# Kernel optimization log

Hardware: AMD Instinct MI355X
Metric: run time of the kernel (lower is better)

The kernel has to match this reference:

```python
import jax, jax.numpy as jnp
import numpy as np

B, C, V = 65536, 2, 3          # batch of coords, coord_dim, value_dim
D, K, S = 64, 1024, 4          # latent_dim, num_codes, num_latent_vectors (VQ stages)
H, L, F = 1024, 5, 25          # hidden_size, num_layers, num_freqs
IN = C * (2 * F + 1)           # 102: positional-encoded decoder input
COMMIT = 0.25


def setup_inputs() -> dict:
    key = jax.random.key(0)
    ks = jax.random.split(key, 12)
    coords = jax.random.uniform(ks[0], (B, C), jnp.float32, -1.0, 1.0)
    latents = jax.random.normal(ks[1], (1, S, D), jnp.float32)
    cb = jax.random.normal(ks[2], (S, K, D), jnp.float32)
    codebooks = cb / jnp.linalg.norm(cb, axis=-1, keepdims=True)  # unit-norm init as in module
    mod_W = jax.random.normal(ks[3], (L, D, H), jnp.float32) / np.sqrt(D)
    mod_b = jax.random.normal(ks[4], (L, H), jnp.float32) * 0.01
    dec_W0 = jax.random.normal(ks[5], (IN, H), jnp.float32) / np.sqrt(IN)
    dec_b0 = jax.random.normal(ks[6], (H,), jnp.float32) * 0.01
    dec_Wh = jax.random.normal(ks[7], (L - 1, H, H), jnp.float32) / np.sqrt(H)
    dec_bh = jax.random.normal(ks[8], (L - 1, H), jnp.float32) * 0.01
    dec_Wout = jax.random.normal(ks[9], (H, V), jnp.float32) / np.sqrt(H)
    dec_bout = jax.random.normal(ks[10], (V,), jnp.float32) * 0.01
    return dict(coords=coords, latent_idx=0, latents=latents, codebooks=codebooks,
                mod_W=mod_W, mod_b=mod_b, dec_W0=dec_W0, dec_b0=dec_b0,
                dec_Wh=dec_Wh, dec_bh=dec_bh, dec_Wout=dec_Wout, dec_bout=dec_bout)


def _vq(z, emb):
    # z: (1, D), emb: (K, D) -> squared-distance argmin + straight-through
    d = jnp.sum(z * z, axis=1, keepdims=True) - 2.0 * (z @ emb.T) + jnp.sum(emb * emb, axis=1)
    idx = jnp.argmin(d, axis=1)               # (1,)
    z_q = emb[idx]                            # (1, D)
    z_q_st = z_q + jax.lax.stop_gradient(z - z_q)   # fwd value == z, grad flows to embedding
    loss = COMMIT * jnp.mean((jax.lax.stop_gradient(z_q) - z) ** 2)
    return z_q_st, idx, loss


def reference(coords, latent_idx, latents, codebooks, mod_W, mod_b,
              dec_W0, dec_b0, dec_Wh, dec_bh, dec_Wout, dec_bout):
    img = latents[latent_idx]                 # (S, D)
    z_q_sum = jnp.zeros((1, D), coords.dtype)
    residual_target = jnp.zeros((1, D), coords.dtype)
    total_vq_loss = 0.0
    idxs = []
    for s in range(S):                        # residual VQ over fixed small #stages
        z_stage = img[s:s + 1]
        if s == 0:
            residual_target = z_stage
            z_cur = z_stage
        else:
            residual_target = residual_target + z_stage
            z_cur = residual_target - jax.lax.stop_gradient(z_q_sum)
        z_q_st, idx, l = _vq(z_cur, codebooks[s])
        z_q_sum = z_q_sum + z_q_st
        total_vq_loss = total_vq_loss + l
        idxs.append(idx)
    # modulation betas from the (same-for-all-rows) quantized latent; broadcast over B
    betas = jnp.einsum('od,ldh->loh', z_q_sum, mod_W) + mod_b[:, None, :]   # (L, 1, H)
    # positional encoding: [x, sin(pi*f0*x), cos(pi*f0*x), sin(pi*f1*x), ...]
    freqs = 2.0 ** jnp.arange(F, dtype=coords.dtype)
    ang = coords[:, None, :] * (freqs[None, :, None] * jnp.pi)              # (B, F, C)
    pe = jnp.concatenate(
        [coords, jnp.stack([jnp.sin(ang), jnp.cos(ang)], axis=2).reshape(coords.shape[0], -1)],
        axis=-1)                                                            # (B, IN)
    h = jax.nn.relu(pe @ dec_W0 + dec_b0 + betas[0])
    for i in range(L - 1):
        h = jax.nn.relu(h @ dec_Wh[i] + dec_bh[i] + betas[i + 1])
    values = h @ dec_Wout + dec_bout                                        # (B, V)
    return values, jnp.stack(idxs), total_vq_loss
```

## Files before the change

### kernel.cpp

```cpp
#include <hip/hip_runtime.h>
#include <hip/hip_bf16.h>
#include <stdint.h>

#define NB   65536
#define NC   2
#define NV   3
#define ND   64
#define NK   1024
#define NS   4
#define NH   1024
#define NL   5
#define NF   25
#define NIN  102
#define K0P  128

typedef float f32x4 __attribute__((ext_vector_type(4)));
typedef int   i32x4 __attribute__((ext_vector_type(4)));
typedef int   i32x8 __attribute__((ext_vector_type(8)));
typedef unsigned char u8;

__device__ __forceinline__ void load_lds16(const void* g, void* l) {
    __builtin_amdgcn_global_load_lds(
        (const __attribute__((address_space(1))) void*)g,
        (__attribute__((address_space(3))) void*)l,
        16, 0, 0);
}

__device__ __forceinline__ u8 to_fp8(float x) {
    return (u8)(__builtin_amdgcn_cvt_pk_fp8_f32(x, 0.0f, 0, false) & 0xff);
}


__global__ __launch_bounds__(1024) void vq_kernel(
    const float* __restrict__ latents, const int* __restrict__ latent_idx,
    const float* __restrict__ codebooks, float* __restrict__ zq_out,
    float* __restrict__ out) {
    __shared__ float zcur[ND], resid[ND], zqsum[ND], ssq[ND];
    __shared__ float sDw[16];
    __shared__ int   sKw[16];
    __shared__ int   sBest;
    int t = threadIdx.x, lane = t & 63, wv = t >> 6;
    const float* img = latents + (size_t)latent_idx[0] * (NS * ND);
    if (t < ND) { resid[t] = 0.f; zqsum[t] = 0.f; }
    __syncthreads();
    float lossAcc = 0.f;
    for (int s = 0; s < NS; s++) {
        if (t < ND) {
            float iv = img[s * ND + t];
            float r  = resid[t] + iv;
            resid[t] = r;
            zcur[t]  = (s == 0) ? iv : (r - zqsum[t]);
        }
        __syncthreads();
        float zz = 0.f;
#pragma unroll
        for (int d = 0; d < ND; d++) { float z = zcur[d]; zz += z * z; }
        const float4* e4 = (const float4*)(codebooks + ((size_t)s * NK + t) * ND);
        float dot = 0.f, ee = 0.f;
#pragma unroll
        for (int i = 0; i < 16; i++) {
            float4 v = e4[i];
            dot += zcur[4 * i + 0] * v.x; dot += zcur[4 * i + 1] * v.y;
            dot += zcur[4 * i + 2] * v.z; dot += zcur[4 * i + 3] * v.w;
            ee  += v.x * v.x; ee += v.y * v.y; ee += v.z * v.z; ee += v.w * v.w;
        }
        float dmin = zz - 2.0f * dot + ee;
        int   kmin = t;
#pragma unroll
        for (int m = 1; m < 64; m <<= 1) {
            float d2 = __shfl_xor(dmin, m);
            int   k2 = __shfl_xor(kmin, m);
            if (d2 < dmin || (d2 == dmin && k2 < kmin)) { dmin = d2; kmin = k2; }
        }
        if (lane == 0) { sDw[wv] = dmin; sKw[wv] = kmin; }
        __syncthreads();
        if (t == 0) {
            float bd = sDw[0]; int bk = sKw[0];
            for (int w = 1; w < 16; w++) {
                float d2 = sDw[w]; int k2 = sKw[w];
                if (d2 < bd || (d2 == bd && k2 < bk)) { bd = d2; bk = k2; }
            }
            sBest = bk;
            out[NB * NV + s] = (float)bk;
        }
        __syncthreads();
        int best = sBest;
        const float* eb = codebooks + ((size_t)s * NK + best) * ND;
        if (t < ND) {
            float zq = eb[t];
            float d  = zq - zcur[t];
            ssq[t]   = d * d;
            zqsum[t] = zqsum[t] + (zq + (zcur[t] - zq));
        }
        __syncthreads();
        if (t == 0) {
            float sum = 0.f;
            for (int d = 0; d < ND; d++) sum += ssq[d];
            lossAcc += 0.25f * (sum / (float)ND);
        }
    }
    if (t < ND) zq_out[t] = zqsum[t];
    if (t == 0) out[NB * NV + NS] = lossAcc;
}

__global__ __launch_bounds__(256) void betas_kernel(
    const float* __restrict__ zq, const float* __restrict__ mod_W,
    const float* __restrict__ mod_b, const float* __restrict__ b0,
    const float* __restrict__ bh, float* __restrict__ bb) {
    int g = blockIdx.x * 256 + threadIdx.x;
    int l = g >> 10, n = g & 1023;
    float acc = mod_b[g];
    for (int d = 0; d < ND; d++) acc += zq[d] * mod_W[(size_t)(l * ND + d) * NH + n];
    acc += (l == 0) ? b0[n] : bh[(size_t)(l - 1) * NH + n];
    bb[g] = acc;
}

__global__ __launch_bounds__(256) void init_out_kernel(
    const float* __restrict__ bout, float* __restrict__ out) {
    int g = blockIdx.x * 256 + threadIdx.x;
    out[g] = bout[g % NV];
}

__global__ __launch_bounds__(256) void prep_kernel(
    const float* __restrict__ src, u8* __restrict__ dst, int Ks, int Kp) {
    __shared__ float tile[32][33];
    int nIt = Kp >> 7;
    src += (size_t)blockIdx.z * Ks * NH;
    dst += (size_t)blockIdx.z * NH * Kp;
    int k0 = blockIdx.x * 32, n0 = blockIdx.y * 32;
    int tx = threadIdx.x, ty = threadIdx.y;
    for (int i = 0; i < 4; i++) {
        int k = k0 + ty + i * 8;
        int n = n0 + tx;
        tile[ty + i * 8][tx] = (k < Ks) ? src[(size_t)k * NH + n] : 0.0f;
    }
    __syncthreads();
    for (int i = 0; i < 4; i++) {
        int n = n0 + ty + i * 8;
        int k = k0 + tx;
        int bn = n >> 7, j = (n >> 4) & 7, r16 = n & 15;
        int it = k >> 7, q = (k >> 5) & 3, half = (k >> 4) & 1, b16 = k & 15;
        size_t flat = ((size_t)(((bn * nIt + it) * 8 + j) * 2 + half)) * 1024
                    + (q * 16 + r16) * 16 + b16;
        dst[flat] = to_fp8(tile[tx][ty + i * 8] * 64.0f);
    }
}

__device__ __forceinline__ float pe_val(const float* coords, int m, int k) {
    if (k < 2) return coords[m * 2 + k];
    if (k >= NIN) return 0.0f;
    int u = k - 2;
    int f = u >> 2, r = u & 3;
    float c = coords[m * 2 + (r & 1)];
    float a = c * __builtin_ldexpf(3.14159274101257324f, f);
    return (r < 2) ? sinf(a) : cosf(a);
}

__global__ __launch_bounds__(256) void pe_kernel(
    const float* __restrict__ coords, u8* __restrict__ pe) {
    int g = blockIdx.x * 256 + threadIdx.x;
    int m = g >> 5, k4 = (g & 31) * 4;
    float v0 = pe_val(coords, m, k4 + 0);
    float v1 = pe_val(coords, m, k4 + 1);
    float v2 = pe_val(coords, m, k4 + 2);
    float v3 = pe_val(coords, m, k4 + 3);
    int p = __builtin_amdgcn_cvt_pk_fp8_f32(v0, v1, 0, false);
    p     = __builtin_amdgcn_cvt_pk_fp8_f32(v2, v3, p, true);
    int m16 = m >> 4, r = m & 15, c32 = k4 >> 5, b = k4 & 31;
    *(int*)(pe + ((size_t)(m16 * 4 + c32) * 16 + r) * 32 + b) = p;
}

template <int MODE, int KT>
__global__ __launch_bounds__(256, 2) void gemm_kernel(
    const u8* __restrict__ A, const u8* __restrict__ W,
    const float* __restrict__ bb, u8* __restrict__ O,
    const float* __restrict__ Wout, float* __restrict__ out, int Mb) {
    __shared__ __align__(16) u8 smem[32768];
    u8* sW0 = smem;
    u8* sW1 = smem + 16384;
    int t   = threadIdx.x;
    int fid = blockIdx.x;
    int xcd = fid & 7;
    int j8  = fid >> 3;
    int bn  = j8 & 7;
    int bm  = xcd * (Mb >> 3) + (j8 >> 3);
    int lane = t & 63, wm = t >> 6;
    int q    = lane >> 4, r16 = lane & 15;
    const int nIt = KT >> 7;

    const u8* wslab = W + (size_t)(bn * nIt) * 16384;
    const u8* abase = A + ((size_t)(bm * 16 + wm * 4) * (KT >> 5)) * 512 + lane * 32;

    f32x4 acc[4][8];
    f32x4 zero = {0.f, 0.f, 0.f, 0.f};
    for (int i = 0; i < 4; i++)
        for (int j = 0; j < 8; j++) acc[i][j] = zero;

#pragma unroll
    for (int p = 0; p < 4; p++) {
        int g = p * 256 + t;
        load_lds16((const void*)(wslab + g * 16), (void*)(sW0 + g * 16));
    }
    i32x8 afc[4], afn[4];
#pragma unroll
    for (int i = 0; i < 4; i++) {
        const u8* p = abase + ((size_t)i * (KT >> 5)) * 512;
        i32x4 lo = *(const i32x4*)(p);
        i32x4 hi = *(const i32x4*)(p + 16);
        afc[i] = __builtin_shufflevector(lo, hi, 0, 1, 2, 3, 4, 5, 6, 7);
    }
    __syncthreads();

#pragma unroll 1
    for (int it = 0; it < nIt; it++) {
        u8* bufc = (it & 1) ? sW1 : sW0;
        u8* bufn = (it & 1) ? sW0 : sW1;
        if (it + 1 < nIt) {
            const u8* ws = wslab + (size_t)(it + 1) * 16384;
#pragma unroll
            for (int p = 0; p < 4; p++) {
                int g = p * 256 + t;
                load_lds16((const void*)(ws + g * 16), (void*)(bufn + g * 16));
            }
#pragma unroll
            for (int i = 0; i < 4; i++) {
                const u8* p = abase + ((size_t)i * (KT >> 5) + (it + 1) * 4) * 512;
                i32x4 lo = *(const i32x4*)(p);
                i32x4 hi = *(const i32x4*)(p + 16);
                afn[i] = __builtin_shufflevector(lo, hi, 0, 1, 2, 3, 4, 5, 6, 7);
            }
        }
#pragma unroll
        for (int j = 0; j < 8; j++) {
            i32x4 lo = *(const i32x4*)(bufc + j * 2048 + lane * 16);
            i32x4 hi = *(const i32x4*)(bufc + j * 2048 + 1024 + lane * 16);
            i32x8 bfr = __builtin_shufflevector(lo, hi, 0, 1, 2, 3, 4, 5, 6, 7);
#pragma unroll
            for (int i = 0; i < 4; i++)
                acc[i][j] = __builtin_amdgcn_mfma_scale_f32_16x16x128_f8f6f4(
                    bfr, afc[i], acc[i][j], 0, 0,
                    0, 0x79797979,
                    0, 0x7f7f7f7f);
        }
        __syncthreads();
#pragma unroll
        for (int i = 0; i < 4; i++) afc[i] = afn[i];
    }

    if constexpr (MODE == 0) {
        u8* eb = smem;
#pragma unroll
        for (int i = 0; i < 4; i++) {
#pragma unroll
            for (int j = 0; j < 8; j++) {
                int nl = j * 16 + q * 4;
                f32x4 b4 = *(const f32x4*)(bb + bn * 128 + nl);
                float v0 = fmaxf(acc[i][j][0] + b4[0], 0.0f);
                float v1 = fmaxf(acc[i][j][1] + b4[1], 0.0f);
                float v2 = fmaxf(acc[i][j][2] + b4[2], 0.0f);
                float v3 = fmaxf(acc[i][j][3] + b4[3], 0.0f);
                int p = __builtin_amdgcn_cvt_pk_fp8_f32(v0, v1, 0, false);
                p     = __builtin_amdgcn_cvt_pk_fp8_f32(v2, v3, p, true);
                int idx = (((wm * 4 + i) * 4 + (j >> 1)) * 16 + r16) * 32
                        + (j & 1) * 16 + q * 4;
                *(int*)(eb + idx) = p;
            }
        }
        __syncthreads();
#pragma unroll
        for (int rd = 0; rd < 8; rd++) {
            int g2  = rd * 256 + t;
            int seg = g2 >> 5, off = (g2 & 31) * 16;
            int m16l = seg >> 2, c32l = seg & 3;
            i32x4 v = *(const i32x4*)(eb + seg * 512 + off);
            *(i32x4*)(O + ((size_t)((bm * 16 + m16l) * 32 + bn * 4 + c32l)) * 512 + off) = v;
        }
    } else {
#pragma unroll
        for (int i = 0; i < 4; i++) {
            float p0 = 0.f, p1 = 0.f, p2 = 0.f;
#pragma unroll
            for (int j = 0; j < 8; j++) {
                int nb = bn * 128 + j * 16 + q * 4;
                f32x4 b4 = *(const f32x4*)(bb + nb);
#pragma unroll
                for (int r = 0; r < 4; r++) {
                    float val = fmaxf(acc[i][j][r] + b4[r], 0.0f);
                    const float* w = Wout + (size_t)(nb + r) * NV;
                    p0 += val * w[0]; p1 += val * w[1]; p2 += val * w[2];
                }
            }
            p0 += __shfl_xor(p0, 16); p0 += __shfl_xor(p0, 32);
            p1 += __shfl_xor(p1, 16); p1 += __shfl_xor(p1, 32);
            p2 += __shfl_xor(p2, 16); p2 += __shfl_xor(p2, 32);
            if (q == 0) {
                int m = bm * 256 + wm * 64 + i * 16 + r16;
                atomicAdd(&out[(size_t)m * NV + 0], p0);
                atomicAdd(&out[(size_t)m * NV + 1], p1);
                atomicAdd(&out[(size_t)m * NV + 2], p2);
            }
        }
    }
}

extern "C" void kernel_launch(void* const* d_in, const int* in_sizes, int n_in,
                              void* d_out, int out_size, void* d_ws, size_t ws_size,
                              hipStream_t stream) {
    const float* coords     = (const float*)d_in[0];
    const int*   latent_idx = (const int*)d_in[1];
    const float* latents    = (const float*)d_in[2];
    const float* codebooks  = (const float*)d_in[3];
    const float* mod_W      = (const float*)d_in[4];
    const float* mod_b      = (const float*)d_in[5];
    const float* dec_W0     = (const float*)d_in[6];
    const float* dec_b0     = (const float*)d_in[7];
    const float* dec_Wh     = (const float*)d_in[8];
    const float* dec_bh     = (const float*)d_in[9];
    const float* dec_Wout   = (const float*)d_in[10];
    const float* dec_bout   = (const float*)d_in[11];
    float* out = (float*)d_out;

    char* wsb = (char*)d_ws;
    float* zq  = (float*)(wsb + 0);
    float* bb  = (float*)(wsb + 256);
    u8*    W0T = (u8*)(wsb + 20736);
    u8*    WhT = (u8*)(wsb + 151808);
    const size_t fixed_end = 4346368;

    int Bc = 65536;
    while (Bc > 2048 && fixed_end + 2 * (size_t)Bc * NH > ws_size)
        Bc >>= 1;
    int Mb = Bc / 256;

    u8* hA = (u8*)(wsb + fixed_end);
    u8* hB = hA + (size_t)Bc * NH;
    u8* pe = hB;

    vq_kernel<<<1, 1024, 0, stream>>>(latents, latent_idx, codebooks, zq, out);
    betas_kernel<<<20, 256, 0, stream>>>(zq, mod_W, mod_b, dec_b0, dec_bh, bb);
    init_out_kernel<<<(NB * NV) / 256, 256, 0, stream>>>(dec_bout, out);
    prep_kernel<<<dim3(4, 32, 1), dim3(32, 8), 0, stream>>>(dec_W0, W0T, NIN, K0P);
    prep_kernel<<<dim3(32, 32, 4), dim3(32, 8), 0, stream>>>(dec_Wh, WhT, NH, NH);

    for (int c0 = 0; c0 < NB; c0 += Bc) {
        pe_kernel<<<(Bc * 32) / 256, 256, 0, stream>>>(coords + (size_t)c0 * NC, pe);
        gemm_kernel<0, K0P><<<8 * Mb, 256, 0, stream>>>(
            pe, W0T, bb + 0 * NH, hA, nullptr, nullptr, Mb);
        gemm_kernel<0, NH><<<8 * Mb, 256, 0, stream>>>(
            hA, WhT + 0 * (size_t)NH * NH, bb + 1 * NH, hB, nullptr, nullptr, Mb);
        gemm_kernel<0, NH><<<8 * Mb, 256, 0, stream>>>(
            hB, WhT + 1 * (size_t)NH * NH, bb + 2 * NH, hA, nullptr, nullptr, Mb);
        gemm_kernel<0, NH><<<8 * Mb, 256, 0, stream>>>(
            hA, WhT + 2 * (size_t)NH * NH, bb + 3 * NH, hB, nullptr, nullptr, Mb);
        gemm_kernel<1, NH><<<8 * Mb, 256, 0, stream>>>(
            hB, WhT + 3 * (size_t)NH * NH, bb + 4 * NH, nullptr,
            dec_Wout, out + (size_t)c0 * NV, Mb);
    }
}
```

Before: 486.8 us.

## Triple-buffer weight tiles with interleaved loads, per-step barriers, and MFMA priority

Replaces the double-buffered LDS weight pipeline with a three-buffer rotation that prefetches two K-tiles ahead. The next activation fragments and the following weight tile are loaded inside the MFMA j-loop, interleaved with the compute. Explicit vmcnt waits replace __syncthreads, and the loop is fully unrolled with register ping-pong. Each j step is bracketed by s_barrier with raised s_setprio around the MFMAs, which aims to overlap global-to-LDS traffic with matrix math. In exchange, LDS use grows to 48KB, which may limit occupancy at 2 blocks per CU, the extra barriers add overhead, and the hand-counted vmcnt values are fragile.

```diff
diff --git a/kernel.cpp b/kernel.cpp
--- a/kernel.cpp
+++ b/kernel.cpp
@@ -175,9 +175,7 @@
     const u8* __restrict__ A, const u8* __restrict__ W,
     const float* __restrict__ bb, u8* __restrict__ O,
     const float* __restrict__ Wout, float* __restrict__ out, int Mb) {
-    __shared__ __align__(16) u8 smem[32768];
-    u8* sW0 = smem;
-    u8* sW1 = smem + 16384;
+    __shared__ __align__(16) u8 smem[49152];
     int t   = threadIdx.x;
     int fid = blockIdx.x;
     int xcd = fid & 7;
@@ -186,7 +184,7 @@
     int bm  = xcd * (Mb >> 3) + (j8 >> 3);
     int lane = t & 63, wm = t >> 6;
     int q    = lane >> 4, r16 = lane & 15;
-    const int nIt = KT >> 7;
+    constexpr int nIt = KT >> 7;
 
     const u8* wslab = W + (size_t)(bn * nIt) * 16384;
     const u8* abase = A + ((size_t)(bm * 16 + wm * 4) * (KT >> 5)) * 512 + lane * 32;
@@ -196,55 +194,81 @@
     for (int i = 0; i < 4; i++)
         for (int j = 0; j < 8; j++) acc[i][j] = zero;
 
+    u8* b0 = smem;
+    u8* b1 = smem + 16384;
+    u8* b2 = smem + 32768;
+
 #pragma unroll
     for (int p = 0; p < 4; p++) {
         int g = p * 256 + t;
-        load_lds16((const void*)(wslab + g * 16), (void*)(sW0 + g * 16));
-    }
-    i32x8 afc[4], afn[4];
+        load_lds16((const void*)(wslab + g * 16), (void*)(b0 + g * 16));
+    }
+    if constexpr (nIt > 1) {
+#pragma unroll
+        for (int p = 0; p < 4; p++) {
+            int g = p * 256 + t;
+            load_lds16((const void*)(wslab + 16384 + g * 16), (void*)(b1 + g * 16));
+        }
+    }
+    i32x8 afA[4], afB[4];
 #pragma unroll
     for (int i = 0; i < 4; i++) {
         const u8* p = abase + ((size_t)i * (KT >> 5)) * 512;
         i32x4 lo = *(const i32x4*)(p);
         i32x4 hi = *(const i32x4*)(p + 16);
-        afc[i] = __builtin_shufflevector(lo, hi, 0, 1, 2, 3, 4, 5, 6, 7);
-    }
-    __syncthreads();
-
-#pragma unroll 1
-    for (int it = 0; it < nIt; it++) {
-        u8* bufc = (it & 1) ? sW1 : sW0;
-        u8* bufn = (it & 1) ? sW0 : sW1;
-        if (it + 1 < nIt) {
-            const u8* ws = wslab + (size_t)(it + 1) * 16384;
-#pragma unroll
-            for (int p = 0; p < 4; p++) {
-                int g = p * 256 + t;
-                load_lds16((const void*)(ws + g * 16), (void*)(bufn + g * 16));
-            }
-#pragma unroll
-            for (int i = 0; i < 4; i++) {
-                const u8* p = abase + ((size_t)i * (KT >> 5) + (it + 1) * 4) * 512;
-                i32x4 lo = *(const i32x4*)(p);
-                i32x4 hi = *(const i32x4*)(p + 16);
-                afn[i] = __builtin_shufflevector(lo, hi, 0, 1, 2, 3, 4, 5, 6, 7);
-            }
-        }
+        afA[i] = __builtin_shufflevector(lo, hi, 0, 1, 2, 3, 4, 5, 6, 7);
+    }
+    if constexpr (nIt > 1) {
+        asm volatile("s_waitcnt vmcnt(4)" ::: "memory");
+    } else {
+        asm volatile("s_waitcnt vmcnt(0)" ::: "memory");
+    }
+    __builtin_amdgcn_s_barrier();
+    asm volatile("" ::: "memory");
+
+    auto ITER = [&](int it, i32x8* afc, i32x8* afn) {
+        const u8* ws = wslab + (size_t)(it + 2) * 16384;
+        const bool haveA = (it + 1 < nIt);
+        const bool haveW = (it + 2 < nIt);
 #pragma unroll
         for (int j = 0; j < 8; j++) {
-            i32x4 lo = *(const i32x4*)(bufc + j * 2048 + lane * 16);
-            i32x4 hi = *(const i32x4*)(bufc + j * 2048 + 1024 + lane * 16);
+            i32x4 lo = *(const i32x4*)(b0 + j * 2048 + lane * 16);
+            i32x4 hi = *(const i32x4*)(b0 + j * 2048 + 1024 + lane * 16);
             i32x8 bfr = __builtin_shufflevector(lo, hi, 0, 1, 2, 3, 4, 5, 6, 7);
+            if (j < 4) {
+                if (haveA) {
+                    const u8* p = abase + ((size_t)j * (KT >> 5) + (it + 1) * 4) * 512;
+                    i32x4 alo = *(const i32x4*)(p);
+                    i32x4 ahi = *(const i32x4*)(p + 16);
+                    afn[j] = __builtin_shufflevector(alo, ahi, 0, 1, 2, 3, 4, 5, 6, 7);
+                }
+            } else if (haveW) {
+                int g = (j - 4) * 256 + t;
+                load_lds16((const void*)(ws + g * 16), (void*)(b2 + g * 16));
+            }
+            __builtin_amdgcn_s_barrier();
+            __builtin_amdgcn_s_setprio(1);
 #pragma unroll
             for (int i = 0; i < 4; i++)
                 acc[i][j] = __builtin_amdgcn_mfma_scale_f32_16x16x128_f8f6f4(
                     bfr, afc[i], acc[i][j], 0, 0,
                     0, 0x79797979,
                     0, 0x7f7f7f7f);
-        }
-        __syncthreads();
-#pragma unroll
-        for (int i = 0; i < 4; i++) afc[i] = afn[i];
+            __builtin_amdgcn_s_setprio(0);
+            if (j == 7 && haveA) {
+                if (haveW) asm volatile("s_waitcnt vmcnt(4)" ::: "memory");
+                else       asm volatile("s_waitcnt vmcnt(0)" ::: "memory");
+            }
+            __builtin_amdgcn_s_barrier();
+            if (j == 7) asm volatile("" ::: "memory");
+        }
+        u8* tmp = b0; b0 = b1; b1 = b2; b2 = tmp;
+    };
+
+#pragma unroll
+    for (int it = 0; it < nIt; it += 2) {
+        ITER(it, afA, afB);
+        if (it + 1 < nIt) ITER(it + 1, afB, afA);
     }
 
     if constexpr (MODE == 0) {
```

After: 513.3 us. +5.4%, slower.

## Triple-buffer weight tiles with fully unrolled interleaved prefetch and per-MFMA barriers

Applied to the files above, without the earlier changes.

Replaces the double-buffered K loop with a three-stage LDS ring (48 KB) that prefetches weight tiles two iterations ahead, and fully unrolls the loop for KT=1024. Global loads for A and W are spread across the j sub-steps between MFMA groups, and explicit vmcnt waits replace the blanket syncthreads. s_setprio is raised around the MFMAs. This aims to hide global-load latency better, but adds two barriers per j step and more LDS, which may reduce occupancy below the two blocks per CU requested by launch bounds.

```diff
diff --git a/kernel.cpp b/kernel.cpp
--- a/kernel.cpp
+++ b/kernel.cpp
@@ -175,9 +175,7 @@
     const u8* __restrict__ A, const u8* __restrict__ W,
     const float* __restrict__ bb, u8* __restrict__ O,
     const float* __restrict__ Wout, float* __restrict__ out, int Mb) {
-    __shared__ __align__(16) u8 smem[32768];
-    u8* sW0 = smem;
-    u8* sW1 = smem + 16384;
+    __shared__ __align__(16) u8 smem[49152];
     int t   = threadIdx.x;
     int fid = blockIdx.x;
     int xcd = fid & 7;
@@ -186,7 +184,7 @@
     int bm  = xcd * (Mb >> 3) + (j8 >> 3);
     int lane = t & 63, wm = t >> 6;
     int q    = lane >> 4, r16 = lane & 15;
-    const int nIt = KT >> 7;
+    constexpr int nIt = KT >> 7;
 
     const u8* wslab = W + (size_t)(bn * nIt) * 16384;
     const u8* abase = A + ((size_t)(bm * 16 + wm * 4) * (KT >> 5)) * 512 + lane * 32;
@@ -199,53 +197,90 @@
 #pragma unroll
     for (int p = 0; p < 4; p++) {
         int g = p * 256 + t;
-        load_lds16((const void*)(wslab + g * 16), (void*)(sW0 + g * 16));
-    }
-    i32x8 afc[4], afn[4];
+        load_lds16((const void*)(wslab + g * 16), (void*)(smem + g * 16));
+    }
+    asm volatile("" ::: "memory");
+    if constexpr (nIt > 1) {
+#pragma unroll
+        for (int p = 0; p < 4; p++) {
+            int g = p * 256 + t;
+            load_lds16((const void*)(wslab + 16384 + g * 16),
+                       (void*)(smem + 16384 + g * 16));
+        }
+        asm volatile("" ::: "memory");
+    }
+    i32x8 afA[4], afB[4];
 #pragma unroll
     for (int i = 0; i < 4; i++) {
         const u8* p = abase + ((size_t)i * (KT >> 5)) * 512;
         i32x4 lo = *(const i32x4*)(p);
         i32x4 hi = *(const i32x4*)(p + 16);
-        afc[i] = __builtin_shufflevector(lo, hi, 0, 1, 2, 3, 4, 5, 6, 7);
-    }
-    __syncthreads();
-
-#pragma unroll 1
-    for (int it = 0; it < nIt; it++) {
-        u8* bufc = (it & 1) ? sW1 : sW0;
-        u8* bufn = (it & 1) ? sW0 : sW1;
-        if (it + 1 < nIt) {
-            const u8* ws = wslab + (size_t)(it + 1) * 16384;
-#pragma unroll
-            for (int p = 0; p < 4; p++) {
-                int g = p * 256 + t;
-                load_lds16((const void*)(ws + g * 16), (void*)(bufn + g * 16));
-            }
-#pragma unroll
-            for (int i = 0; i < 4; i++) {
-                const u8* p = abase + ((size_t)i * (KT >> 5) + (it + 1) * 4) * 512;
-                i32x4 lo = *(const i32x4*)(p);
-                i32x4 hi = *(const i32x4*)(p + 16);
-                afn[i] = __builtin_shufflevector(lo, hi, 0, 1, 2, 3, 4, 5, 6, 7);
-            }
-        }
-#pragma unroll
-        for (int j = 0; j < 8; j++) {
-            i32x4 lo = *(const i32x4*)(bufc + j * 2048 + lane * 16);
-            i32x4 hi = *(const i32x4*)(bufc + j * 2048 + 1024 + lane * 16);
-            i32x8 bfr = __builtin_shufflevector(lo, hi, 0, 1, 2, 3, 4, 5, 6, 7);
-#pragma unroll
-            for (int i = 0; i < 4; i++)
-                acc[i][j] = __builtin_amdgcn_mfma_scale_f32_16x16x128_f8f6f4(
-                    bfr, afc[i], acc[i][j], 0, 0,
-                    0, 0x79797979,
-                    0, 0x7f7f7f7f);
-        }
-        __syncthreads();
-#pragma unroll
-        for (int i = 0; i < 4; i++) afc[i] = afn[i];
-    }
+        afA[i] = __builtin_shufflevector(lo, hi, 0, 1, 2, 3, 4, 5, 6, 7);
+    }
+    if constexpr (nIt > 1) {
+        asm volatile("s_waitcnt vmcnt(12)" ::: "memory");
+    } else {
+        asm volatile("s_waitcnt vmcnt(0)" ::: "memory");
+    }
+    __builtin_amdgcn_s_barrier();
+    asm volatile("" ::: "memory");
+
+#define GEMM_ITER(IT, CB, SB, AFC, AFN, HA, HW)                               \
+    {                                                                          \
+        _Pragma("unroll")                                                      \
+        for (int j = 0; j < 8; j++) {                                          \
+            i32x4 lo = *(const i32x4*)(smem + (CB) * 16384 + j * 2048          \
+                                       + lane * 16);                           \
+            i32x4 hi = *(const i32x4*)(smem + (CB) * 16384 + j * 2048 + 1024   \
+                                       + lane * 16);                           \
+            i32x8 bfr = __builtin_shufflevector(lo, hi, 0, 1, 2, 3, 4, 5, 6, 7);\
+            if (j < 4) {                                                       \
+                if (HA) {                                                      \
+                    const u8* p = abase                                        \
+                        + ((size_t)j * (KT >> 5) + ((IT) + 1) * 4) * 512;      \
+                    i32x4 alo = *(const i32x4*)(p);                            \
+                    i32x4 ahi = *(const i32x4*)(p + 16);                       \
+                    AFN[j] = __builtin_shufflevector(alo, ahi,                 \
+                                                     0, 1, 2, 3, 4, 5, 6, 7); \
+                }                                                              \
+            } else if (HW) {                                                   \
+                int g = (j - 4) * 256 + t;                                     \
+                load_lds16((const void*)(wslab + (size_t)((IT) + 2) * 16384    \
+                                         + g * 16),                            \
+                           (void*)(smem + (SB) * 16384 + g * 16));             \
+            }                                                                  \
+            __builtin_amdgcn_s_barrier();                                      \
+            __builtin_amdgcn_s_setprio(1);                                     \
+            _Pragma("unroll")                                                  \
+            for (int i = 0; i < 4; i++)                                        \
+                acc[i][j] = __builtin_amdgcn_mfma_scale_f32_16x16x128_f8f6f4(  \
+                    bfr, AFC[i], acc[i][j], 0, 0,                              \
+                    0, 0x79797979,                   \
+                    0, 0x7f7f7f7f);                  \
+            __builtin_amdgcn_s_setprio(0);                                     \
+            if (j == 7 && (HA)) {                                              \
+                if (HW) asm volatile("s_waitcnt vmcnt(4)" ::: "memory");       \
+                else    asm volatile("s_waitcnt vmcnt(0)" ::: "memory");       \
+            }                                                                  \
+            __builtin_amdgcn_s_barrier();                                      \
+            if (j == 3 || j == 7) asm volatile("" ::: "memory");               \
+        }                                                                      \
+    }
+
+    if constexpr (nIt == 8) {
+        GEMM_ITER(0, 0, 2, afA, afB, true,  true)
+        GEMM_ITER(1, 1, 0, afB, afA, true,  true)
+        GEMM_ITER(2, 2, 1, afA, afB, true,  true)
+        GEMM_ITER(3, 0, 2, afB, afA, true,  true)
+        GEMM_ITER(4, 1, 0, afA, afB, true,  true)
+        GEMM_ITER(5, 2, 1, afB, afA, true,  true)
+        GEMM_ITER(6, 0, 2, afA, afB, true,  false)
+        GEMM_ITER(7, 1, 0, afB, afA, false, false)
+    } else {
+        static_assert(KT == K0P, "unexpected KT");
+        GEMM_ITER(0, 0, 1, afA, afB, false, false)
+    }
+#undef GEMM_ITER
 
     if constexpr (MODE == 0) {
         u8* eb = smem;
```

After: 514.9 us. +5.8%, slower.

## Restructure fp8 GEMM into 8-wave triple-buffered LDS pipeline with staged A tiles

Applied to the files above, without the earlier changes.

The decoder GEMM moves from 4 waves that each hold A fragments in registers and double-buffer only the weights to 8 waves in a 2x4 layout. Both A and W tiles are staged into LDS with direct global-to-LDS loads through a 3-buffer, 144 KB pipeline, with explicit vmcnt waits, barriers and setprio around the MFMA bursts. The final layer reduces its per-wave output partials in LDS before issuing atomics, which cuts the atomic count. The aim is better overlap of memory and MFMA work and less register pressure, at the cost of large LDS use that may limit occupancy to one block per CU.

```diff
diff --git a/kernel.cpp b/kernel.cpp
--- a/kernel.cpp
+++ b/kernel.cpp
@@ -28,6 +28,13 @@
 
 __device__ __forceinline__ u8 to_fp8(float x) {
     return (u8)(__builtin_amdgcn_cvt_pk_fp8_f32(x, 0.0f, 0, false) & 0xff);
+}
+
+__device__ __forceinline__ f32x4 mfma128(i32x8 wf, i32x8 af, f32x4 c) {
+    return __builtin_amdgcn_mfma_scale_f32_16x16x128_f8f6f4(
+        wf, af, c, 0, 0,
+        0, 0x79797979,
+        0, 0x7f7f7f7f);
 }
 
 
@@ -171,136 +178,222 @@
 }
 
 template <int MODE, int KT>
-__global__ __launch_bounds__(256, 2) void gemm_kernel(
+__global__ __launch_bounds__(512, 2) void gemm_kernel(
     const u8* __restrict__ A, const u8* __restrict__ W,
     const float* __restrict__ bb, u8* __restrict__ O,
     const float* __restrict__ Wout, float* __restrict__ out, int Mb) {
-    __shared__ __align__(16) u8 smem[32768];
-    u8* sW0 = smem;
-    u8* sW1 = smem + 16384;
+    extern __shared__ __align__(16) u8 smem[];
     int t   = threadIdx.x;
     int fid = blockIdx.x;
     int xcd = fid & 7;
     int j8  = fid >> 3;
     int bn  = j8 & 7;
     int bm  = xcd * (Mb >> 3) + (j8 >> 3);
-    int lane = t & 63, wm = t >> 6;
+    int lane = t & 63, w = t >> 6;
+    int wm2  = w >> 2, wn = w & 3;
     int q    = lane >> 4, r16 = lane & 15;
-    const int nIt = KT >> 7;
+    constexpr int nIt = KT >> 7;
+    constexpr int KC  = KT >> 5;
 
     const u8* wslab = W + (size_t)(bn * nIt) * 16384;
-    const u8* abase = A + ((size_t)(bm * 16 + wm * 4) * (KT >> 5)) * 512 + lane * 32;
-
-    f32x4 acc[4][8];
+
+    f32x4 acc[8][2];
     f32x4 zero = {0.f, 0.f, 0.f, 0.f};
-    for (int i = 0; i < 4; i++)
-        for (int j = 0; j < 8; j++) acc[i][j] = zero;
-
-#pragma unroll
-    for (int p = 0; p < 4; p++) {
-        int g = p * 256 + t;
-        load_lds16((const void*)(wslab + g * 16), (void*)(sW0 + g * 16));
-    }
-    i32x8 afc[4], afn[4];
-#pragma unroll
-    for (int i = 0; i < 4; i++) {
-        const u8* p = abase + ((size_t)i * (KT >> 5)) * 512;
-        i32x4 lo = *(const i32x4*)(p);
-        i32x4 hi = *(const i32x4*)(p + 16);
-        afc[i] = __builtin_shufflevector(lo, hi, 0, 1, 2, 3, 4, 5, 6, 7);
-    }
-    __syncthreads();
-
-#pragma unroll 1
-    for (int it = 0; it < nIt; it++) {
-        u8* bufc = (it & 1) ? sW1 : sW0;
-        u8* bufn = (it & 1) ? sW0 : sW1;
-        if (it + 1 < nIt) {
-            const u8* ws = wslab + (size_t)(it + 1) * 16384;
-#pragma unroll
-            for (int p = 0; p < 4; p++) {
-                int g = p * 256 + t;
-                load_lds16((const void*)(ws + g * 16), (void*)(bufn + g * 16));
-            }
-#pragma unroll
-            for (int i = 0; i < 4; i++) {
-                const u8* p = abase + ((size_t)i * (KT >> 5) + (it + 1) * 4) * 512;
-                i32x4 lo = *(const i32x4*)(p);
-                i32x4 hi = *(const i32x4*)(p + 16);
-                afn[i] = __builtin_shufflevector(lo, hi, 0, 1, 2, 3, 4, 5, 6, 7);
-            }
-        }
-#pragma unroll
-        for (int j = 0; j < 8; j++) {
-            i32x4 lo = *(const i32x4*)(bufc + j * 2048 + lane * 16);
-            i32x4 hi = *(const i32x4*)(bufc + j * 2048 + 1024 + lane * 16);
-            i32x8 bfr = __builtin_shufflevector(lo, hi, 0, 1, 2, 3, 4, 5, 6, 7);
-#pragma unroll
-            for (int i = 0; i < 4; i++)
-                acc[i][j] = __builtin_amdgcn_mfma_scale_f32_16x16x128_f8f6f4(
-                    bfr, afc[i], acc[i][j], 0, 0,
-                    0, 0x79797979,
-                    0, 0x7f7f7f7f);
-        }
-        __syncthreads();
-#pragma unroll
-        for (int i = 0; i < 4; i++) afc[i] = afn[i];
-    }
+    for (int i = 0; i < 8; i++) { acc[i][0] = zero; acc[i][1] = zero; }
+
+#define FENCE asm volatile("" ::: "memory")
+
+#define STAGE_A(B, IT, CC)                                                     \
+    {                                                                          \
+        int lc = w * 8 + (CC) * 2 + (lane >> 5);                               \
+        load_lds16((const void*)(A + ((size_t)(bm * 16 + (lc >> 2)) * KC       \
+                                      + (IT) * 4 + (lc & 3)) * 512             \
+                                 + (lane & 31) * 16),                          \
+                   (void*)(smem + (B) * 49152 + (w * 8 + (CC) * 2) * 512       \
+                           + lane * 16));                                      \
+    }
+#define STAGE_W(B, IT, CC)                                                     \
+    {                                                                          \
+        int off = (w * 2 + (CC)) * 1024 + lane * 16;                           \
+        load_lds16((const void*)(wslab + (size_t)(IT) * 16384 + off),          \
+                   (void*)(smem + (B) * 49152 + 32768 + off));                 \
+    }
+#define LDPAIR(dst, base, d)                                                   \
+    {                                                                          \
+        i32x4 lo_ = *(const i32x4*)(base);                                     \
+        i32x4 hi_ = *(const i32x4*)((base) + (d));                             \
+        dst = __builtin_shufflevector(lo_, hi_, 0, 1, 2, 3, 4, 5, 6, 7);       \
+    }
+
+    if constexpr (nIt > 1) {
+        STAGE_A(0, 0, 0) STAGE_A(0, 0, 1) STAGE_A(0, 0, 2) STAGE_A(0, 0, 3)
+        STAGE_W(0, 0, 0) STAGE_W(0, 0, 1)
+        FENCE;
+        STAGE_A(1, 1, 0) STAGE_A(1, 1, 1) STAGE_A(1, 1, 2) STAGE_A(1, 1, 3)
+        STAGE_W(1, 1, 0) STAGE_W(1, 1, 1)
+        FENCE;
+        asm volatile("s_waitcnt vmcnt(6)" ::: "memory");
+    } else {
+        STAGE_A(0, 0, 0) STAGE_A(0, 0, 1) STAGE_A(0, 0, 2) STAGE_A(0, 0, 3)
+        STAGE_W(0, 0, 0) STAGE_W(0, 0, 1)
+        FENCE;
+        asm volatile("s_waitcnt vmcnt(0)" ::: "memory");
+    }
+    __builtin_amdgcn_s_barrier();
+
+#define GEMM_ITER(IT, CB, SB, HA, HW)                                          \
+    {                                                                          \
+        const u8* Ab = smem + (CB) * 49152;                                    \
+        const u8* Wb = Ab + 32768;                                             \
+        i32x8 bf0, bf1;                                                        \
+        LDPAIR(bf0, Wb + (wn * 2 + 0) * 2048 + lane * 16, 1024)                \
+        LDPAIR(bf1, Wb + (wn * 2 + 1) * 2048 + lane * 16, 1024)                \
+        {                                                                      \
+            i32x8 a0, a1, a2, a3;                                              \
+            LDPAIR(a0, Ab + (wm2 * 8 + 0) * 2048 + lane * 32, 16)              \
+            LDPAIR(a1, Ab + (wm2 * 8 + 1) * 2048 + lane * 32, 16)              \
+            LDPAIR(a2, Ab + (wm2 * 8 + 2) * 2048 + lane * 32, 16)              \
+            LDPAIR(a3, Ab + (wm2 * 8 + 3) * 2048 + lane * 32, 16)              \
+            if (HW) {                                                          \
+                FENCE;                                                         \
+                STAGE_A(SB, (IT) + 2, 0) STAGE_A(SB, (IT) + 2, 1)              \
+                STAGE_W(SB, (IT) + 2, 0)                                       \
+                FENCE;                                                         \
+            }                                                                  \
+            __builtin_amdgcn_s_barrier();                                      \
+            __builtin_amdgcn_s_setprio(1);                                     \
+            acc[0][0] = mfma128(bf0, a0, acc[0][0]);                           \
+            acc[0][1] = mfma128(bf1, a0, acc[0][1]);                           \
+            acc[1][0] = mfma128(bf0, a1, acc[1][0]);                           \
+            acc[1][1] = mfma128(bf1, a1, acc[1][1]);                           \
+            acc[2][0] = mfma128(bf0, a2, acc[2][0]);                           \
+            acc[2][1] = mfma128(bf1, a2, acc[2][1]);                           \
+            acc[3][0] = mfma128(bf0, a3, acc[3][0]);                           \
+            acc[3][1] = mfma128(bf1, a3, acc[3][1]);                           \
+            __builtin_amdgcn_s_setprio(0);                                     \
+            __builtin_amdgcn_s_barrier();                                      \
+        }                                                                      \
+        {                                                                      \
+            i32x8 a4, a5, a6, a7;                                              \
+            LDPAIR(a4, Ab + (wm2 * 8 + 4) * 2048 + lane * 32, 16)              \
+            LDPAIR(a5, Ab + (wm2 * 8 + 5) * 2048 + lane * 32, 16)              \
+            LDPAIR(a6, Ab + (wm2 * 8 + 6) * 2048 + lane * 32, 16)              \
+            LDPAIR(a7, Ab + (wm2 * 8 + 7) * 2048 + lane * 32, 16)              \
+            if (HW) {                                                          \
+                FENCE;                                                         \
+                STAGE_A(SB, (IT) + 2, 2) STAGE_A(SB, (IT) + 2, 3)              \
+                STAGE_W(SB, (IT) + 2, 1)                                       \
+                FENCE;                                                         \
+            }                                                                  \
+            __builtin_amdgcn_s_barrier();                                      \
+            __builtin_amdgcn_s_setprio(1);                                     \
+            acc[4][0] = mfma128(bf0, a4, acc[4][0]);                           \
+            acc[4][1] = mfma128(bf1, a4, acc[4][1]);                           \
+            acc[5][0] = mfma128(bf0, a5, acc[5][0]);                           \
+            acc[5][1] = mfma128(bf1, a5, acc[5][1]);                           \
+            acc[6][0] = mfma128(bf0, a6, acc[6][0]);                           \
+            acc[6][1] = mfma128(bf1, a6, acc[6][1]);                           \
+            acc[7][0] = mfma128(bf0, a7, acc[7][0]);                           \
+            acc[7][1] = mfma128(bf1, a7, acc[7][1]);                           \
+            __builtin_amdgcn_s_setprio(0);                                     \
+            if (HA) {                                                          \
+                if (HW) asm volatile("s_waitcnt vmcnt(6)" ::: "memory");       \
+                else    asm volatile("s_waitcnt vmcnt(0)" ::: "memory");       \
+            }                                                                  \
+            __builtin_amdgcn_s_barrier();                                      \
+        }                                                                      \
+    }
+
+    if constexpr (nIt == 8) {
+        GEMM_ITER(0, 0, 2, true,  true)
+        GEMM_ITER(1, 1, 0, true,  true)
+        GEMM_ITER(2, 2, 1, true,  true)
+        GEMM_ITER(3, 0, 2, true,  true)
+        GEMM_ITER(4, 1, 0, true,  true)
+        GEMM_ITER(5, 2, 1, true,  true)
+        GEMM_ITER(6, 0, 2, true,  false)
+        GEMM_ITER(7, 1, 0, false, false)
+    } else {
+        static_assert(KT == K0P, "unexpected KT");
+        GEMM_ITER(0, 0, 0, false, false)
+    }
+#undef GEMM_ITER
+#undef STAGE_A
+#undef STAGE_W
+#undef LDPAIR
 
     if constexpr (MODE == 0) {
+        __syncthreads();
         u8* eb = smem;
 #pragma unroll
-        for (int i = 0; i < 4; i++) {
-#pragma unroll
-            for (int j = 0; j < 8; j++) {
-                int nl = j * 16 + q * 4;
+        for (int i = 0; i < 8; i++) {
+#pragma unroll
+            for (int jj = 0; jj < 2; jj++) {
+                int nl = wn * 32 + jj * 16 + q * 4;
                 f32x4 b4 = *(const f32x4*)(bb + bn * 128 + nl);
-                float v0 = fmaxf(acc[i][j][0] + b4[0], 0.0f);
-                float v1 = fmaxf(acc[i][j][1] + b4[1], 0.0f);
-                float v2 = fmaxf(acc[i][j][2] + b4[2], 0.0f);
-                float v3 = fmaxf(acc[i][j][3] + b4[3], 0.0f);
+                float v0 = fmaxf(acc[i][jj][0] + b4[0], 0.0f);
+                float v1 = fmaxf(acc[i][jj][1] + b4[1], 0.0f);
+                float v2 = fmaxf(acc[i][jj][2] + b4[2], 0.0f);
+                float v3 = fmaxf(acc[i][jj][3] + b4[3], 0.0f);
                 int p = __builtin_amdgcn_cvt_pk_fp8_f32(v0, v1, 0, false);
                 p     = __builtin_amdgcn_cvt_pk_fp8_f32(v2, v3, p, true);
-                int idx = (((wm * 4 + i) * 4 + (j >> 1)) * 16 + r16) * 32
-                        + (j & 1) * 16 + q * 4;
+                int m16l = wm2 * 8 + i;
+                int idx = ((m16l * 4 + wn) * 16 + r16) * 32 + jj * 16 + q * 4;
                 *(int*)(eb + idx) = p;
             }
         }
         __syncthreads();
 #pragma unroll
-        for (int rd = 0; rd < 8; rd++) {
-            int g2  = rd * 256 + t;
+        for (int rd = 0; rd < 4; rd++) {
+            int g2  = rd * 512 + t;
             int seg = g2 >> 5, off = (g2 & 31) * 16;
-            int m16l = seg >> 2, c32l = seg & 3;
             i32x4 v = *(const i32x4*)(eb + seg * 512 + off);
-            *(i32x4*)(O + ((size_t)((bm * 16 + m16l) * 32 + bn * 4 + c32l)) * 512 + off) = v;
+            *(i32x4*)(O + ((size_t)((bm * 16 + (seg >> 2)) * 32 + bn * 4
+                                    + (seg & 3))) * 512 + off) = v;
         }
     } else {
-#pragma unroll
-        for (int i = 0; i < 4; i++) {
+        __syncthreads();
+        float* red = (float*)smem;
+#pragma unroll
+        for (int i = 0; i < 8; i++) {
             float p0 = 0.f, p1 = 0.f, p2 = 0.f;
 #pragma unroll
-            for (int j = 0; j < 8; j++) {
-                int nb = bn * 128 + j * 16 + q * 4;
+            for (int jj = 0; jj < 2; jj++) {
+                int nb = bn * 128 + wn * 32 + jj * 16 + q * 4;
                 f32x4 b4 = *(const f32x4*)(bb + nb);
 #pragma unroll
                 for (int r = 0; r < 4; r++) {
-                    float val = fmaxf(acc[i][j][r] + b4[r], 0.0f);
-                    const float* w = Wout + (size_t)(nb + r) * NV;
-                    p0 += val * w[0]; p1 += val * w[1]; p2 += val * w[2];
+                    float val = fmaxf(acc[i][jj][r] + b4[r], 0.0f);
+                    const float* wo = Wout + (size_t)(nb + r) * NV;
+                    p0 += val * wo[0]; p1 += val * wo[1]; p2 += val * wo[2];
                 }
             }
             p0 += __shfl_xor(p0, 16); p0 += __shfl_xor(p0, 32);
             p1 += __shfl_xor(p1, 16); p1 += __shfl_xor(p1, 32);
             p2 += __shfl_xor(p2, 16); p2 += __shfl_xor(p2, 32);
             if (q == 0) {
-                int m = bm * 256 + wm * 64 + i * 16 + r16;
-                atomicAdd(&out[(size_t)m * NV + 0], p0);
-                atomicAdd(&out[(size_t)m * NV + 1], p1);
-                atomicAdd(&out[(size_t)m * NV + 2], p2);
+                int row = (wm2 * 8 + i) * 16 + r16;
+                int base = (row * 4 + wn) * 3;
+                red[base + 0] = p0; red[base + 1] = p1; red[base + 2] = p2;
             }
         }
-    }
+        __syncthreads();
+        if (t < 256) {
+            int row = t;
+            float s0 = 0.f, s1 = 0.f, s2 = 0.f;
+#pragma unroll
+            for (int c = 0; c < 4; c++) {
+                s0 += red[(row * 4 + c) * 3 + 0];
+                s1 += red[(row * 4 + c) * 3 + 1];
+                s2 += red[(row * 4 + c) * 3 + 2];
+            }
+            int m = bm * 256 + row;
+            atomicAdd(&out[(size_t)m * NV + 0], s0);
+            atomicAdd(&out[(size_t)m * NV + 1], s1);
+            atomicAdd(&out[(size_t)m * NV + 2], s2);
+        }
+    }
+#undef FENCE
 }
 
 extern "C" void kernel_launch(void* const* d_in, const int* in_sizes, int n_in,
@@ -336,6 +429,14 @@
     u8* hB = hA + (size_t)Bc * NH;
     u8* pe = hB;
 
+    const int LDS_BYTES = 147456;
+    hipFuncSetAttribute(reinterpret_cast<const void*>(gemm_kernel<0, K0P>),
+                        hipFuncAttributeMaxDynamicSharedMemorySize, LDS_BYTES);
+    hipFuncSetAttribute(reinterpret_cast<const void*>(gemm_kernel<0, NH>),
+                        hipFuncAttributeMaxDynamicSharedMemorySize, LDS_BYTES);
+    hipFuncSetAttribute(reinterpret_cast<const void*>(gemm_kernel<1, NH>),
+                        hipFuncAttributeMaxDynamicSharedMemorySize, LDS_BYTES);
+
     vq_kernel<<<1, 1024, 0, stream>>>(latents, latent_idx, codebooks, zq, out);
     betas_kernel<<<20, 256, 0, stream>>>(zq, mod_W, mod_b, dec_b0, dec_bh, bb);
     init_out_kernel<<<(NB * NV) / 256, 256, 0, stream>>>(dec_bout, out);
@@ -344,15 +445,15 @@
 
     for (int c0 = 0; c0 < NB; c0 += Bc) {
         pe_kernel<<<(Bc * 32) / 256, 256, 0, stream>>>(coords + (size_t)c0 * NC, pe);
-        gemm_kernel<0, K0P><<<8 * Mb, 256, 0, stream>>>(
+        gemm_kernel<0, K0P><<<8 * Mb, 512, LDS_BYTES, stream>>>(
             pe, W0T, bb + 0 * NH, hA, nullptr, nullptr, Mb);
-        gemm_kernel<0, NH><<<8 * Mb, 256, 0, stream>>>(
+        gemm_kernel<0, NH><<<8 * Mb, 512, LDS_BYTES, stream>>>(
             hA, WhT + 0 * (size_t)NH * NH, bb + 1 * NH, hB, nullptr, nullptr, Mb);
-        gemm_kernel<0, NH><<<8 * Mb, 256, 0, stream>>>(
+        gemm_kernel<0, NH><<<8 * Mb, 512, LDS_BYTES, stream>>>(
             hB, WhT + 1 * (size_t)NH * NH, bb + 2 * NH, hA, nullptr, nullptr, Mb);
-        gemm_kernel<0, NH><<<8 * Mb, 256, 0, stream>>>(
+        gemm_kernel<0, NH><<<8 * Mb, 512, LDS_BYTES, stream>>>(
             hA, WhT + 2 * (size_t)NH * NH, bb + 3 * NH, hB, nullptr, nullptr, Mb);
-        gemm_kernel<1, NH><<<8 * Mb, 256, 0, stream>>>(
+        gemm_kernel<1, NH><<<8 * Mb, 512, LDS_BYTES, stream>>>(
             hB, WhT + 3 * (size_t)NH * NH, bb + 4 * NH, nullptr,
             dec_Wout, out + (size_t)c0 * NV, Mb);
     }
```

Measured after the change: 691.8 us. +42.1%, slower.
